# Kernel optimization log

Measured on AMD Instinct MI355X. Metric: run time of the kernel, lower is better.

The kernel has to match this reference:

```python
import jax, jax.numpy as jnp
import numpy as np

B, D_IN, D_OUT, DICT = 2048, 768, 768, 24576
TOP_K, TOP_K_AUX = 32, 512
L1_COEFF, AUX_PENALTY, N_DEAD = 0.001, 0.03125, 100.0


def setup_inputs() -> dict:
    key = jax.random.key(0)
    k1, k2, k3, k4, k5, k6 = jax.random.split(key, 6)
    x_in = jax.random.normal(k1, (B, D_IN), dtype=jnp.float32)
    y_target = jax.random.normal(k2, (B, D_OUT), dtype=jnp.float32)
    nb = jax.random.randint(k3, (DICT,), 0, 200).astype(jnp.float32)
    # kaiming-uniform-ish init
    bound_e = float(np.sqrt(6.0 / D_IN))
    W_enc = jax.random.uniform(k4, (D_IN, DICT), minval=-bound_e, maxval=bound_e, dtype=jnp.float32)
    bound_d = float(np.sqrt(6.0 / DICT))
    W_dec = jax.random.uniform(k5, (DICT, D_OUT), minval=-bound_d, maxval=bound_d, dtype=jnp.float32)
    W_dec = W_dec / jnp.linalg.norm(W_dec, axis=-1, keepdims=True)  # unit-norm rows
    b_dec = jnp.zeros((D_OUT,), dtype=jnp.float32)
    return {"x_in": x_in, "y_target": y_target, "num_batches_not_active": nb,
            "W_enc": W_enc, "W_dec": W_dec, "b_dec": b_dec}


def _unit_norm(x):
    m = x.mean(axis=-1, keepdims=True)
    x = x - m
    s = jnp.std(x, axis=-1, keepdims=True, ddof=1)  # torch .std is unbiased
    return x / (s + 1e-5), m, s


def reference(x_in, y_target, num_batches_not_active, W_enc, W_dec, b_dec):
    xn, _, _ = _unit_norm(x_in)
    yn, y_mean, y_std = _unit_norm(y_target)
    x_enc = xn - b_dec  # pre_enc_bias (input_size == output_size)
    acts = jax.nn.relu(x_enc @ W_enc)                      # [B, DICT]
    vals, idx = jax.lax.top_k(acts, TOP_K)                 # [B, TOP_K]
    rows = jnp.arange(B)[:, None]
    acts_sparse = jnp.zeros_like(acts).at[rows, idx].set(vals)
    y_pred = acts_sparse @ W_dec + b_dec                   # [B, D_OUT]
    y_pred_out = y_pred * y_std + y_mean

    # stateful dead-feature bookkeeping (update_inactive_features)
    col_active = acts_sparse.sum(axis=0) > 0
    nb = jnp.where(col_active, 0.0, num_batches_not_active + 1.0)

    l2_loss = jnp.mean((y_pred - yn) ** 2)
    l1_norm = jnp.mean(jnp.abs(acts_sparse).sum(axis=-1))
    l1_loss = L1_COEFF * l1_norm
    l0_norm = jnp.mean((acts_sparse > 0).astype(jnp.float32).sum(axis=-1))

    # auxiliary loss on dead features (static-shape masked top-k; masked cols
    # get -1 < relu acts so extras relu-clip to 0 -> same math as torch gather)
    dead = nb >= N_DEAD
    masked = jnp.where(dead[None, :], acts, -1.0)
    av, ai = jax.lax.top_k(masked, TOP_K_AUX)
    av = jax.nn.relu(av)
    acts_aux = jnp.zeros_like(acts).at[rows, ai].set(av)
    y_pred_aux = acts_aux @ W_dec
    residual = yn - y_pred
    l2_aux = AUX_PENALTY * jnp.mean((y_pred_aux - residual) ** 2)
    aux_loss = jnp.where(dead.any(), l2_aux, 0.0)

    loss = l2_loss + l1_loss + aux_loss
    num_dead_features = (nb > N_DEAD).sum()
    return (y_pred_out, acts_sparse, loss, l2_loss, l1_loss, l0_norm, l1_norm,
            aux_loss, num_dead_features)
```

## Files before the change

### kernel.cpp

```cpp
#include <hip/hip_runtime.h>
#include <math.h>

#define BATCH 2048
#define DIN 768
#define DICT 24576
#define KM 32
#define KA 512
#define NPT 48
#define L1_COEFF 0.001f
#define AUX_PENALTY 0.03125f
#define CAND_MAX 128
#define CAND_DELTA 0.08f
#define AUX_SPLIT 8
#define SAUX 18432
#define AGB ((DIN/128)*(BATCH/128)*AUX_SPLIT)

typedef __attribute__((ext_vector_type(8))) short bf16x8;
typedef __attribute__((ext_vector_type(8))) unsigned short u16x8;
typedef __attribute__((ext_vector_type(4))) float f32x4;

constexpr size_t WS_XENC   = 0;
constexpr size_t WS_YN     = WS_XENC + (size_t)BATCH*DIN;
constexpr size_t WS_YMEAN  = WS_YN + (size_t)BATCH*DIN;
constexpr size_t WS_YSTD   = WS_YMEAN + BATCH;
constexpr size_t WS_RES    = WS_YSTD + BATCH;
constexpr size_t WS_NSEL   = WS_RES + (size_t)BATCH*DIN;
constexpr size_t WS_SEL    = WS_NSEL + BATCH;
constexpr size_t WS_SELV   = WS_SEL + (size_t)BATCH*KM;
constexpr size_t WS_COLACT = WS_SELV + (size_t)BATCH*KM;
constexpr size_t WS_ACC    = WS_COLACT + DICT;
constexpr size_t WS_DB     = WS_ACC + 8;
constexpr size_t WS_XEB    = WS_DB + DICT/32;
constexpr size_t WS_WETF   = WS_XEB + (size_t)BATCH*DIN/2;
constexpr size_t WS_WETB   = WS_WETF + (size_t)DICT*DIN;
constexpr size_t WS_WDB    = WS_WETB + (size_t)DICT*DIN/2;
constexpr size_t WS_DPREF  = WS_XEB + DICT/32;
constexpr size_t WS_META   = WS_XEB + 2*(DICT/32);

__device__ __forceinline__ unsigned short f2b(float f){
    unsigned u = __float_as_uint(f);
    return (unsigned short)((u + 0x7fffu + ((u >> 16) & 1u)) >> 16);
}
__device__ __forceinline__ float b2f(unsigned short h){ return __uint_as_float(((unsigned)h) << 16); }

__device__ __forceinline__ void gld_lds16(const void* g, void* l){
    __builtin_amdgcn_global_load_lds(
        (const __attribute__((address_space(1))) unsigned int*)g,
        (__attribute__((address_space(3))) unsigned int*)l, 16, 0, 0);
}

__device__ __forceinline__ int blk_count512_w(int cw, int* s16, int par){
    if ((threadIdx.x & 63) == 0) s16[par*8 + (threadIdx.x >> 6)] = cw;
    __syncthreads();
    int tot = 0;
    #pragma unroll
    for (int w=0; w<8; w++) tot += s16[par*8+w];
    return tot;
}
__device__ __forceinline__ float blk_sum512(float v, float* s16, int par){
    #pragma unroll
    for (int off=32; off; off>>=1) v += __shfl_down(v, off);
    if ((threadIdx.x & 63) == 0) s16[par*8 + (threadIdx.x >> 6)] = v;
    __syncthreads();
    float t = 0.f;
    #pragma unroll
    for (int w=0; w<8; w++) t += s16[par*8+w];
    return t;
}
__device__ __forceinline__ float blk_sum256(float v, float* s8, int par){
    #pragma unroll
    for (int off=32; off; off>>=1) v += __shfl_down(v, off);
    if ((threadIdx.x & 63) == 0) s8[par*4 + (threadIdx.x >> 6)] = v;
    __syncthreads();
    float t = 0.f;
    #pragma unroll
    for (int w=0; w<4; w++) t += s8[par*4+w];
    return t;
}

__global__ __launch_bounds__(256) void prep_k(const float* __restrict__ x,
        const float* __restrict__ y, const float* __restrict__ bdec,
        const float* __restrict__ We, const float* __restrict__ Wd,
        float* __restrict__ Tf, unsigned short* __restrict__ Tb,
        unsigned short* __restrict__ Td, float* __restrict__ ws){
    __shared__ float s8[8];
    __shared__ float t1[32][33];
    __shared__ float t2[32][33];
    const int tid = threadIdx.x;
    if (blockIdx.x < 2*BATCH){
        int b = blockIdx.x; bool isy = b >= BATCH; int row = isy ? b - BATCH : b;
        if (b < 8){
            float* dst = ws + WS_COLACT;
            for (int i = b*256 + tid; i < DICT + 8; i += 2048) dst[i] = 0.f;
        }
        const float* src = (isy ? y : x) + (size_t)row*DIN;
        float v0 = src[tid], v1 = src[tid+256], v2 = src[tid+512];
        float s = blk_sum256(v0+v1+v2, s8, 0);
        float mean = s * (1.f/(float)DIN);
        float d0 = v0-mean, d1 = v1-mean, d2 = v2-mean;
        float vs = blk_sum256(d0*d0+d1*d1+d2*d2, s8, 1);
        float sd = sqrtf(vs / (float)(DIN-1));
        float inv = 1.f / (sd + 1e-5f);
        if (isy){
            float* yn = ws + WS_YN + (size_t)row*DIN;
            yn[tid] = d0*inv; yn[tid+256] = d1*inv; yn[tid+512] = d2*inv;
            if (tid==0){ ws[WS_YMEAN+row] = mean; ws[WS_YSTD+row] = sd; }
        } else {
            float* xe = ws + WS_XENC + (size_t)row*DIN;
            unsigned short* xeb = (unsigned short*)(ws + WS_XEB) + (size_t)row*DIN;
            float e0 = d0*inv - bdec[tid];
            float e1 = d1*inv - bdec[tid+256];
            float e2 = d2*inv - bdec[tid+512];
            xe[tid] = e0; xe[tid+256] = e1; xe[tid+512] = e2;
            xeb[tid] = f2b(e0); xeb[tid+256] = f2b(e1); xeb[tid+512] = f2b(e2);
        }
    } else {
        int t = blockIdx.x - 2*BATCH;
        int bx = t % (DICT/32), by = t / (DICT/32);
        int a0 = bx*32, k0 = by*32;
        int r = tid >> 5, c = tid & 31;
        #pragma unroll
        for (int rr=r; rr<32; rr+=8){
            t1[rr][c] = We[(size_t)(k0+rr)*DICT + a0 + c];
            t2[rr][c] = Wd[(size_t)(a0+rr)*DIN + k0 + c];
        }
        __syncthreads();
        #pragma unroll
        for (int rr=r; rr<32; rr+=8){
            float v = t1[c][rr];
            Tf[(size_t)(a0+rr)*DIN + k0 + c] = v;
            Tb[(size_t)(a0+rr)*DIN + k0 + c] = f2b(v);
            Td[(size_t)(k0+rr)*DICT + a0 + c] = f2b(t2[c][rr]);
        }
    }
}

__global__ __launch_bounds__(256) void gemm_mfma(const unsigned short* __restrict__ Abf,
        const unsigned short* __restrict__ Bbf, unsigned short* __restrict__ C){
    __shared__ __align__(16) unsigned short As[128*64];
    __shared__ __align__(16) unsigned short Bs[128*64];
    const int tid = threadIdx.x;
    const int w = tid >> 6, lane = tid & 63;
    const int g = blockIdx.x;
    const int xcd = g & 7;
    const int s_ = g >> 3;
    const int m_t = s_ & 15;
    const int n_t = xcd + 8*(s_ >> 4);
    const int m0 = m_t*128, n0 = n_t*128;
    const int srow = lane >> 3;
    const int schunk = (lane & 7) ^ srow;
    const int wm = (w >> 1)*64, wn = (w & 1)*64;
    f32x4 acc[16];
    #pragma unroll
    for (int i=0;i<16;i++) acc[i] = (f32x4){0.f,0.f,0.f,0.f};
    for (int kt = 0; kt < DIN; kt += 64){
        #pragma unroll
        for (int q=0;q<4;q++){
            int s = w*4 + q;
            int row = 8*s + srow;
            gld_lds16(Abf + (size_t)(m0+row)*DIN + kt + schunk*8, &As[8*s*64]);
            gld_lds16(Bbf + (size_t)(n0+row)*DIN + kt + schunk*8, &Bs[8*s*64]);
        }
        __syncthreads();
        #pragma unroll
        for (int kk=0; kk<64; kk+=32){
            bf16x8 af[4], bfr[4];
            int ch = (kk>>3) + (lane>>4);
            #pragma unroll
            for (int i=0;i<4;i++){
                int row = wm + i*16 + (lane&15);
                af[i] = *(const bf16x8*)&As[row*64 + ((ch ^ (row&7))<<3)];
            }
            #pragma unroll
            for (int j=0;j<4;j++){
                int row = wn + j*16 + (lane&15);
                bfr[j] = *(const bf16x8*)&Bs[row*64 + ((ch ^ (row&7))<<3)];
            }
            #pragma unroll
            for (int i=0;i<4;i++)
                #pragma unroll
                for (int j=0;j<4;j++)
                    acc[i*4+j] = __builtin_amdgcn_mfma_f32_16x16x32_bf16(af[i], bfr[j], acc[i*4+j], 0,0,0);
        }
        __syncthreads();
    }
    #pragma unroll
    for (int i=0;i<4;i++){
        #pragma unroll
        for (int r=0;r<4;r++){
            int m = m0 + wm + i*16 + (lane>>4)*4 + r;
            unsigned short* crow = C + (size_t)m*DICT + n0 + wn + (lane&15);
            #pragma unroll
            for (int j=0;j<4;j++)
                crow[j*16] = f2b(fmaxf(acc[i*4+j][r], 0.f) + 0.0f);
        }
    }
}

__global__ __launch_bounds__(512) void topk_main(const unsigned short* __restrict__ actsb,
        const float* __restrict__ WeTf, const float* __restrict__ Wdec,
        const float* __restrict__ bdec, float* __restrict__ ws,
        float* __restrict__ ypred_out){
    const int row = blockIdx.x, tid = threadIdx.x;
    const int lane = tid & 63, wid = tid >> 6;
    __shared__ int   s_i16[16];
    __shared__ float s_f16[16];
    __shared__ float s_x[DIN];
    __shared__ int   s_ci[CAND_MAX];
    __shared__ float s_cv[CAND_MAX];
    __shared__ int   s_li[KM];
    __shared__ float s_lv[KM];
    __shared__ int   s_n, s_m;
    const unsigned short* arow = actsb + (size_t)row * DICT;
    float* xrow = ws + WS_XENC + (size_t)row * DIN;
    unsigned short h[NPT];
    #pragma unroll
    for (int i=0;i<6;i++){
        u16x8 v = *(const u16x8*)&arow[i*4096 + tid*8];
        #pragma unroll
        for (int e=0;e<8;e++) h[i*8+e] = v[e];
    }
    s_x[tid] = xrow[tid];
    if (tid < DIN-512) s_x[tid+512] = xrow[tid+512];
    if (tid == 0){ s_n = 0; s_m = 0; }

    int par = 0;
    unsigned prefix = 0;
    for (int bit=14; bit>=0; bit--){
        unsigned cand = prefix | (1u<<bit);
        int c = 0;
        #pragma unroll
        for (int q=0;q<NPT;q++) c += (int)__popcll(__ballot((unsigned)h[q] >= cand));
        int tot = blk_count512_w(c, s_i16, par); par ^= 1;
        if (tot >= KM) prefix = cand;
    }
    float tc = b2f((unsigned short)prefix) - CAND_DELTA;
    #pragma unroll
    for (int q=0;q<NPT;q++){
        if (b2f(h[q]) > tc){
            int p = atomicAdd(&s_n, 1);
            if (p < CAND_MAX) s_ci[p] = (q>>3)*4096 + tid*8 + (q&7);
        }
    }
    __syncthreads();
    int nc = s_n; if (nc > CAND_MAX) nc = CAND_MAX;
    for (int c = wid; c < nc; c += 8){
        const float* wr = WeTf + (size_t)s_ci[c]*DIN;
        float p = 0.f;
        #pragma unroll
        for (int t=0; t<12; t++) p = fmaf(s_x[lane + 64*t], wr[lane + 64*t], p);
        #pragma unroll
        for (int off=32; off; off>>=1) p += __shfl_down(p, off);
        if (lane == 0) s_cv[c] = fmaxf(p, 0.f);
    }
    __syncthreads();
    if (tid < nc){
        float vi = s_cv[tid]; int ii = s_ci[tid];
        int rank = 0;
        for (int j=0; j<nc; j++){
            float vj = s_cv[j];
            rank += (vj > vi) || (vj == vi && s_ci[j] < ii);
        }
        if (rank < KM){
            int p = atomicAdd(&s_m, 1);
            s_li[p] = ii; s_lv[p] = vi;
        }
    }
    __syncthreads();
    if (tid < KM){
        ((int*)ws)[WS_COLACT + s_li[tid]] = 1;
        ((int*)ws)[WS_SEL  + (size_t)row*KM + tid] = s_li[tid];
        ws[WS_SELV + (size_t)row*KM + tid] = s_lv[tid];
    }
    if (tid == 0){
        float l1 = 0.f; int l0 = 0;
        for (int l=0;l<KM;l++){ l1 += s_lv[l]; l0 += (s_lv[l] > 0.f); }
        atomicAdd(&ws[WS_ACC+1], l1);
        atomicAdd(&ws[WS_ACC+2], (float)l0);
    }
    __syncthreads();
    float ym = ws[WS_YMEAN+row], ys = ws[WS_YSTD+row];
    float l2loc = 0.f;
    for (int c = tid; c < DIN; c += 512){
        float acc = bdec[c];
        #pragma unroll 4
        for (int l=0;l<KM;l++) acc = fmaf(s_lv[l], Wdec[(size_t)s_li[l]*DIN + c], acc);
        float ynv = ws[WS_YN + (size_t)row*DIN + c];
        float d = acc - ynv;
        l2loc += d*d;
        ws[WS_RES + (size_t)row*DIN + c] = ynv - acc;
        ypred_out[(size_t)row*DIN + c] = fmaf(acc, ys, ym);
        xrow[c] = 0.f;
    }
    if (tid < DIN-512) xrow[tid+512] = 0.f;
    float l2t = blk_sum512(l2loc, s_f16, 0);
    if (tid==0) atomicAdd(&ws[WS_ACC+0], l2t);
}

__global__ __launch_bounds__(768) void deadscan_k(const float* __restrict__ nb,
        float* __restrict__ ws){
    __shared__ int s[DICT/32];
    __shared__ int c12[12];
    const int t = threadIdx.x;
    const int* colact = (const int*)ws + WS_COLACT;
    unsigned bits = 0; int cgt = 0;
    const int base = t*32;
    #pragma unroll 8
    for (int b=0;b<32;b++){
        int j = base + b;
        float nbn = colact[j] ? 0.f : nb[j] + 1.f;
        bits |= (nbn >= 100.f ? 1u : 0u) << b;
        cgt  += (nbn > 100.f) ? 1 : 0;
    }
    ((unsigned*)(ws + WS_DB))[t] = bits;
    int pc = __popc(bits);
    s[t] = pc;
    #pragma unroll
    for (int off=32; off; off>>=1) cgt += __shfl_down(cgt, off);
    if ((t & 63) == 0) c12[t >> 6] = cgt;
    __syncthreads();
    for (int off=1; off<DICT/32; off<<=1){
        int v = (t >= off) ? s[t-off] : 0;
        __syncthreads();
        s[t] += v;
        __syncthreads();
    }
    ((int*)(ws + WS_DPREF))[t] = s[t] - pc;
    if (t == DICT/32 - 1){
        int nd = s[t];
        int ndpad = (nd + 63) & ~63;
        if (ndpad > SAUX) ndpad = SAUX;
        int* meta = (int*)(ws + WS_META);
        meta[0] = nd; meta[1] = ndpad; meta[2] = ndpad >> 6;
        meta[3] = ((ndpad >> 6) + AUX_SPLIT - 1) / AUX_SPLIT;
        int tot = 0;
        #pragma unroll
        for (int wv=0; wv<12; wv++) tot += c12[wv];
        ws[WS_ACC+4] = (float)tot;
        ((int*)ws)[WS_ACC+5] = (nd > 0) ? 1 : 0;
    }
}

__global__ __launch_bounds__(512) void auxprep_k(const unsigned short* __restrict__ actsb,
        unsigned short* __restrict__ wdt, unsigned short* __restrict__ auxc,
        float* __restrict__ ws){
    __shared__ unsigned s_db[DICT/32];
    __shared__ int      s_dp[DICT/32];
    __shared__ int      s_i16[16];
    const int tid = threadIdx.x;
    for (int i=tid; i<DICT/32; i+=512){
        s_db[i] = ((const unsigned*)(ws + WS_DB))[i];
        s_dp[i] = ((const int*)(ws + WS_DPREF))[i];
    }
    const int nd    = ((const int*)(ws + WS_META))[0];
    const int ndpad = ((const int*)(ws + WS_META))[1];
    __syncthreads();
    if (blockIdx.x < DIN){
        const int n = blockIdx.x;
        unsigned short* row = wdt + (size_t)n*DICT;
        for (int ch = 0; ch < DICT; ch += 4096){
            u16x8 a = *(const u16x8*)&row[ch + tid*8];
            __syncthreads();
            int w = (ch>>5) + (tid>>2);
            unsigned dbw = s_db[w]; int dpw = s_dp[w];
            int bit0 = (tid&3)*8;
            #pragma unroll
            for (int e=0;e<8;e++){
                int bit = bit0 + e;
                if ((dbw >> bit) & 1u)
                    row[dpw + __popc(dbw & ((1u<<bit)-1u))] = a[e];
            }
            __syncthreads();
        }
        for (int t2 = nd + tid; t2 < ndpad; t2 += 512) row[t2] = 0;
    } else {
        const int row = blockIdx.x - DIN;
        const unsigned short* arow = actsb + (size_t)row * DICT;
        unsigned short key[NPT];
        #pragma unroll
        for (int i=0;i<6;i++){
            u16x8 v = *(const u16x8*)&arow[i*4096 + tid*8];
            unsigned dbw = s_db[i*128 + (tid>>2)];
            #pragma unroll
            for (int e=0;e<8;e++){
                unsigned short hv = v[e];
                key[i*8+e] = (((dbw >> ((tid&3)*8 + e)) & 1u) && hv) ? hv : 0;
            }
        }
        int par = 0;
        unsigned prefix = 0;
        for (int bit=14; bit>=0; bit--){
            unsigned cand = prefix | (1u<<bit);
            int c = 0;
            #pragma unroll
            for (int q=0;q<NPT;q++) c += (int)__popcll(__ballot((unsigned)key[q] >= cand));
            int tot = blk_count512_w(c, s_i16, par); par ^= 1;
            if (tot >= KA) prefix = cand;
        }
        unsigned thr = prefix ? prefix : 1u;
        unsigned short* crow = auxc + (size_t)row * SAUX;
        #pragma unroll
        for (int i=0;i<6;i++){
            int w = i*128 + (tid>>2);
            unsigned dbw = s_db[w];
            int dpw = s_dp[w];
            #pragma unroll
            for (int e=0;e<8;e++){
                int bit = (tid&3)*8 + e;
                if ((dbw >> bit) & 1u){
                    int p = dpw + __popc(dbw & ((1u<<bit)-1u));
                    unsigned short kv = key[i*8+e];
                    if (p < SAUX) crow[p] = ((unsigned)kv >= thr) ? kv : (unsigned short)0;
                }
            }
        }
        for (int t2 = nd + tid; t2 < ndpad; t2 += 512) crow[t2] = 0;
    }
}

__global__ __launch_bounds__(256) void auxgz_k(const unsigned short* __restrict__ Abf,
        const unsigned short* __restrict__ Bbf, float* __restrict__ ws,
        float* __restrict__ yaux, float* __restrict__ acts){
    __shared__ __align__(16) unsigned short As[128*64];
    __shared__ __align__(16) unsigned short Bs[128*64];
    const int tid = threadIdx.x;
    if (blockIdx.x >= AGB){
        const int row = blockIdx.x - AGB;
        float4 z = make_float4(0.f,0.f,0.f,0.f);
        float4* arow4 = (float4*)(acts + (size_t)row*DICT);
        #pragma unroll
        for (int i=0;i<24;i++) arow4[tid + 256*i] = z;
        __syncthreads();
        if (tid < KM){
            int j   = ((const int*)ws)[WS_SEL + (size_t)row*KM + tid];
            float v = ws[WS_SELV + (size_t)row*KM + tid];
            (acts + (size_t)row*DICT)[j] = v;
        }
        return;
    }
    const int nkt   = ((const int*)(ws + WS_META))[2];
    const int chunk = ((const int*)(ws + WS_META))[3];
    const int g = blockIdx.x;
    const int z = g & 7;
    const int s_ = g >> 3;
    const int m_t = s_ & 15;
    const int n_t = s_ >> 4;
    int t0 = z * chunk;
    int t1 = t0 + chunk; if (t1 > nkt) t1 = nkt;
    if (t0 >= t1) return;
    const int w = tid >> 6, lane = tid & 63;
    const int m0 = m_t*128, n0 = n_t*128;
    const int srow = lane >> 3;
    const int schunk = (lane & 7) ^ srow;
    const int wm = (w >> 1)*64, wn = (w & 1)*64;
    f32x4 acc[16];
    #pragma unroll
    for (int i=0;i<16;i++) acc[i] = (f32x4){0.f,0.f,0.f,0.f};
    for (int t = t0; t < t1; ++t){
        int kt = t*64;
        #pragma unroll
        for (int q=0;q<4;q++){
            int s = w*4 + q;
            int row = 8*s + srow;
            gld_lds16(Abf + (size_t)(m0+row)*SAUX + kt + schunk*8, &As[8*s*64]);
            gld_lds16(Bbf + (size_t)(n0+row)*DICT + kt + schunk*8, &Bs[8*s*64]);
        }
        __syncthreads();
        #pragma unroll
        for (int kk=0; kk<64; kk+=32){
            bf16x8 af[4], bfr[4];
            int ch = (kk>>3) + (lane>>4);
            #pragma unroll
            for (int i=0;i<4;i++){
                int row = wm + i*16 + (lane&15);
                af[i] = *(const bf16x8*)&As[row*64 + ((ch ^ (row&7))<<3)];
            }
            #pragma unroll
            for (int j=0;j<4;j++){
                int row = wn + j*16 + (lane&15);
                bfr[j] = *(const bf16x8*)&Bs[row*64 + ((ch ^ (row&7))<<3)];
            }
            #pragma unroll
            for (int i=0;i<4;i++)
                #pragma unroll
                for (int j=0;j<4;j++)
                    acc[i*4+j] = __builtin_amdgcn_mfma_f32_16x16x32_bf16(af[i], bfr[j], acc[i*4+j], 0,0,0);
        }
        __syncthreads();
    }
    #pragma unroll
    for (int i=0;i<4;i++){
        #pragma unroll
        for (int r=0;r<4;r++){
            int m = m0 + wm + i*16 + (lane>>4)*4 + r;
            float* crow = yaux + (size_t)m*DIN + n0 + wn + (lane&15);
            #pragma unroll
            for (int j=0;j<4;j++) atomicAdd(&crow[j*16], acc[i*4+j][r]);
        }
    }
}

__global__ __launch_bounds__(256) void auxloss_k(const float* __restrict__ yaux,
        float* __restrict__ ws){
    __shared__ float s8[8];
    const float4* y4 = (const float4*)yaux;
    const float4* r4 = (const float4*)(ws + WS_RES);
    float s = 0.f;
    const size_t n4 = (size_t)BATCH*DIN/4;
    for (size_t i = (size_t)blockIdx.x*256 + threadIdx.x; i < n4; i += (size_t)gridDim.x*256){
        float4 a = y4[i], b = r4[i];
        float d0 = a.x-b.x, d1 = a.y-b.y, d2 = a.z-b.z, d3 = a.w-b.w;
        s += d0*d0 + d1*d1 + d2*d2 + d3*d3;
    }
    float tot = blk_sum256(s, s8, 0);
    if (threadIdx.x == 0) atomicAdd(&ws[WS_ACC+3], tot);
}

__global__ void finalize_k(const float* __restrict__ ws, float* __restrict__ out){
    if (threadIdx.x == 0){
        float l2   = ws[WS_ACC+0] / (float)((size_t)BATCH*DIN);
        float l1n  = ws[WS_ACC+1] / (float)BATCH;
        float l1l  = L1_COEFF * l1n;
        float l0   = ws[WS_ACC+2] / (float)BATCH;
        float auxm = AUX_PENALTY * (ws[WS_ACC+3] / (float)((size_t)BATCH*DIN));
        int any    = ((const int*)ws)[WS_ACC+5];
        float auxl = any ? auxm : 0.f;
        out[0] = l2 + l1l + auxl;
        out[1] = l2;
        out[2] = l1l;
        out[3] = l0;
        out[4] = l1n;
        out[5] = auxl;
        out[6] = ws[WS_ACC+4];
    }
}

extern "C" void kernel_launch(void* const* d_in, const int* in_sizes, int n_in,
                              void* d_out, int out_size, void* d_ws, size_t ws_size,
                              hipStream_t stream){
    const float* x_in = (const float*)d_in[0];
    const float* y_t  = (const float*)d_in[1];
    const float* nb   = (const float*)d_in[2];
    const float* Wenc = (const float*)d_in[3];
    const float* Wdec = (const float*)d_in[4];
    const float* bdec = (const float*)d_in[5];
    float* out  = (float*)d_out;
    float* ws   = (float*)d_ws;
    float* acts = out + (size_t)BATCH*DIN;
    float* scal = out + (size_t)BATCH*DIN + (size_t)BATCH*DICT;
    unsigned short* actsb = (unsigned short*)acts;

    unsigned short* xeb  = (unsigned short*)(ws + WS_XEB);
    float*          wetf = ws + WS_WETF;
    unsigned short* wetb = (unsigned short*)(ws + WS_WETB);
    unsigned short* wdt  = (unsigned short*)(ws + WS_WDB);
    unsigned short* auxc = (unsigned short*)(ws + WS_WETF);
    float*          yaux = ws + WS_XENC;

    prep_k<<<2*BATCH + (DICT/32)*(DIN/32), 256, 0, stream>>>(
        x_in, y_t, bdec, Wenc, Wdec, wetf, wetb, wdt, ws);
    gemm_mfma<<<(DICT/128)*(BATCH/128), 256, 0, stream>>>(xeb, wetb, actsb);
    topk_main<<<BATCH, 512, 0, stream>>>(actsb, wetf, Wdec, bdec, ws, out);
    deadscan_k<<<1, DICT/32, 0, stream>>>(nb, ws);
    auxprep_k<<<DIN + BATCH, 512, 0, stream>>>(actsb, wdt, auxc, ws);
    auxgz_k<<<AGB + BATCH, 256, 0, stream>>>(auxc, wdt, ws, yaux, acts);
    auxloss_k<<<256, 256, 0, stream>>>(yaux, ws);
    finalize_k<<<1, 64, 0, stream>>>(ws, scal);
}
```

Baseline: 858.5 us.

## Stage aux compaction in LDS, replace split-K atomics with partial buffers

The aux GEMM's split-K partial results now go to eight separate workspace buffers with plain stores instead of float atomicAdd. The loss kernel sums the eight partials while reading the residual, which also removes the need to zero the yaux buffer in topk_main. The auxprep compaction of W_dec rows and aux codes is staged in a shared-memory buffer and written out with coalesced vector stores instead of scattered global writes. The main top-k threshold search now counts per wave without a block-wide reduction, and the candidate capacity is raised to 768 to cover the larger candidate set this produces. The cost is more LDS per block and more global traffic in the loss kernel reading eight buffers.

```diff
diff --git a/kernel.cpp b/kernel.cpp
--- a/kernel.cpp
+++ b/kernel.cpp
@@ -9,7 +9,7 @@
 #define NPT 48
 #define L1_COEFF 0.001f
 #define AUX_PENALTY 0.03125f
-#define CAND_MAX 128
+#define CAND_MAX 768
 #define CAND_DELTA 0.08f
 #define AUX_SPLIT 8
 #define SAUX 18432
@@ -203,7 +203,6 @@
         float* __restrict__ ypred_out){
     const int row = blockIdx.x, tid = threadIdx.x;
     const int lane = tid & 63, wid = tid >> 6;
-    __shared__ int   s_i16[16];
     __shared__ float s_f16[16];
     __shared__ float s_x[DIN];
     __shared__ int   s_ci[CAND_MAX];
@@ -212,7 +211,7 @@
     __shared__ float s_lv[KM];
     __shared__ int   s_n, s_m;
     const unsigned short* arow = actsb + (size_t)row * DICT;
-    float* xrow = ws + WS_XENC + (size_t)row * DIN;
+    const float* xrow = ws + WS_XENC + (size_t)row * DIN;
     unsigned short h[NPT];
     #pragma unroll
     for (int i=0;i<6;i++){
@@ -224,17 +223,16 @@
     if (tid < DIN-512) s_x[tid+512] = xrow[tid+512];
     if (tid == 0){ s_n = 0; s_m = 0; }
 
-    int par = 0;
     unsigned prefix = 0;
     for (int bit=14; bit>=0; bit--){
         unsigned cand = prefix | (1u<<bit);
         int c = 0;
         #pragma unroll
         for (int q=0;q<NPT;q++) c += (int)__popcll(__ballot((unsigned)h[q] >= cand));
-        int tot = blk_count512_w(c, s_i16, par); par ^= 1;
-        if (tot >= KM) prefix = cand;
+        if (c >= KM) prefix = cand;
     }
     float tc = b2f((unsigned short)prefix) - CAND_DELTA;
+    __syncthreads();
     #pragma unroll
     for (int q=0;q<NPT;q++){
         if (b2f(h[q]) > tc){
@@ -290,9 +288,7 @@
         l2loc += d*d;
         ws[WS_RES + (size_t)row*DIN + c] = ynv - acc;
         ypred_out[(size_t)row*DIN + c] = fmaf(acc, ys, ym);
-        xrow[c] = 0.f;
-    }
-    if (tid < DIN-512) xrow[tid+512] = 0.f;
+    }
     float l2t = blk_sum512(l2loc, s_f16, 0);
     if (tid==0) atomicAdd(&ws[WS_ACC+0], l2t);
 }
@@ -347,6 +343,7 @@
     __shared__ unsigned s_db[DICT/32];
     __shared__ int      s_dp[DICT/32];
     __shared__ int      s_i16[16];
+    __shared__ unsigned short s_out[SAUX];
     const int tid = threadIdx.x;
     for (int i=tid; i<DICT/32; i+=512){
         s_db[i] = ((const unsigned*)(ws + WS_DB))[i];
@@ -358,21 +355,24 @@
     if (blockIdx.x < DIN){
         const int n = blockIdx.x;
         unsigned short* row = wdt + (size_t)n*DICT;
-        for (int ch = 0; ch < DICT; ch += 4096){
-            u16x8 a = *(const u16x8*)&row[ch + tid*8];
-            __syncthreads();
-            int w = (ch>>5) + (tid>>2);
+        #pragma unroll
+        for (int i=0;i<6;i++){
+            u16x8 a = *(const u16x8*)&row[i*4096 + tid*8];
+            int w = i*128 + (tid>>2);
             unsigned dbw = s_db[w]; int dpw = s_dp[w];
-            int bit0 = (tid&3)*8;
             #pragma unroll
             for (int e=0;e<8;e++){
-                int bit = bit0 + e;
-                if ((dbw >> bit) & 1u)
-                    row[dpw + __popc(dbw & ((1u<<bit)-1u))] = a[e];
-            }
-            __syncthreads();
-        }
-        for (int t2 = nd + tid; t2 < ndpad; t2 += 512) row[t2] = 0;
+                int bit = (tid&3)*8 + e;
+                if ((dbw >> bit) & 1u){
+                    int p = dpw + __popc(dbw & ((1u<<bit)-1u));
+                    if (p < SAUX) s_out[p] = a[e];
+                }
+            }
+        }
+        for (int t2 = nd + tid; t2 < ndpad; t2 += 512) s_out[t2] = 0;
+        __syncthreads();
+        for (int i = tid*8; i < ndpad; i += 4096)
+            *(u16x8*)&row[i] = *(const u16x8*)&s_out[i];
     } else {
         const int row = blockIdx.x - DIN;
         const unsigned short* arow = actsb + (size_t)row * DICT;
@@ -398,7 +398,6 @@
             if (tot >= KA) prefix = cand;
         }
         unsigned thr = prefix ? prefix : 1u;
-        unsigned short* crow = auxc + (size_t)row * SAUX;
         #pragma unroll
         for (int i=0;i<6;i++){
             int w = i*128 + (tid>>2);
@@ -410,17 +409,21 @@
                 if ((dbw >> bit) & 1u){
                     int p = dpw + __popc(dbw & ((1u<<bit)-1u));
                     unsigned short kv = key[i*8+e];
-                    if (p < SAUX) crow[p] = ((unsigned)kv >= thr) ? kv : (unsigned short)0;
+                    if (p < SAUX) s_out[p] = ((unsigned)kv >= thr) ? kv : (unsigned short)0;
                 }
             }
         }
-        for (int t2 = nd + tid; t2 < ndpad; t2 += 512) crow[t2] = 0;
+        for (int t2 = nd + tid; t2 < ndpad; t2 += 512) s_out[t2] = 0;
+        __syncthreads();
+        unsigned short* crow = auxc + (size_t)row * SAUX;
+        for (int i = tid*8; i < ndpad; i += 4096)
+            *(u16x8*)&crow[i] = *(const u16x8*)&s_out[i];
     }
 }
 
 __global__ __launch_bounds__(256) void auxgz_k(const unsigned short* __restrict__ Abf,
         const unsigned short* __restrict__ Bbf, float* __restrict__ ws,
-        float* __restrict__ yaux, float* __restrict__ acts){
+        float* __restrict__ acts){
     __shared__ __align__(16) unsigned short As[128*64];
     __shared__ __align__(16) unsigned short Bs[128*64];
     const int tid = threadIdx.x;
@@ -447,7 +450,6 @@
     const int n_t = s_ >> 4;
     int t0 = z * chunk;
     int t1 = t0 + chunk; if (t1 > nkt) t1 = nkt;
-    if (t0 >= t1) return;
     const int w = tid >> 6, lane = tid & 63;
     const int m0 = m_t*128, n0 = n_t*128;
     const int srow = lane >> 3;
@@ -488,29 +490,42 @@
         }
         __syncthreads();
     }
+    float* buf = ws + ((z < 6) ? (WS_WETB + (size_t)z*BATCH*DIN)
+                               : (z == 6 ? WS_YN : WS_XENC));
     #pragma unroll
     for (int i=0;i<4;i++){
         #pragma unroll
         for (int r=0;r<4;r++){
             int m = m0 + wm + i*16 + (lane>>4)*4 + r;
-            float* crow = yaux + (size_t)m*DIN + n0 + wn + (lane&15);
-            #pragma unroll
-            for (int j=0;j<4;j++) atomicAdd(&crow[j*16], acc[i*4+j][r]);
-        }
-    }
-}
-
-__global__ __launch_bounds__(256) void auxloss_k(const float* __restrict__ yaux,
-        float* __restrict__ ws){
+            float* crow = buf + (size_t)m*DIN + n0 + wn + (lane&15);
+            #pragma unroll
+            for (int j=0;j<4;j++) crow[j*16] = acc[i*4+j][r];
+        }
+    }
+}
+
+__global__ __launch_bounds__(256) void auxloss_k(float* __restrict__ ws){
     __shared__ float s8[8];
-    const float4* y4 = (const float4*)yaux;
+    const float4* b0 = (const float4*)(ws + WS_WETB);
+    const float4* b1 = (const float4*)(ws + WS_WETB + 1*(size_t)BATCH*DIN);
+    const float4* b2 = (const float4*)(ws + WS_WETB + 2*(size_t)BATCH*DIN);
+    const float4* b3 = (const float4*)(ws + WS_WETB + 3*(size_t)BATCH*DIN);
+    const float4* b4 = (const float4*)(ws + WS_WETB + 4*(size_t)BATCH*DIN);
+    const float4* b5 = (const float4*)(ws + WS_WETB + 5*(size_t)BATCH*DIN);
+    const float4* b6 = (const float4*)(ws + WS_YN);
+    const float4* b7 = (const float4*)(ws + WS_XENC);
     const float4* r4 = (const float4*)(ws + WS_RES);
     float s = 0.f;
     const size_t n4 = (size_t)BATCH*DIN/4;
     for (size_t i = (size_t)blockIdx.x*256 + threadIdx.x; i < n4; i += (size_t)gridDim.x*256){
-        float4 a = y4[i], b = r4[i];
-        float d0 = a.x-b.x, d1 = a.y-b.y, d2 = a.z-b.z, d3 = a.w-b.w;
-        s += d0*d0 + d1*d1 + d2*d2 + d3*d3;
+        float4 a0 = b0[i], a1 = b1[i], a2 = b2[i], a3 = b3[i];
+        float4 a4 = b4[i], a5 = b5[i], a6 = b6[i], a7 = b7[i];
+        float4 rr = r4[i];
+        float x0 = ((a0.x+a1.x)+(a2.x+a3.x))+((a4.x+a5.x)+(a6.x+a7.x)) - rr.x;
+        float x1 = ((a0.y+a1.y)+(a2.y+a3.y))+((a4.y+a5.y)+(a6.y+a7.y)) - rr.y;
+        float x2 = ((a0.z+a1.z)+(a2.z+a3.z))+((a4.z+a5.z)+(a6.z+a7.z)) - rr.z;
+        float x3 = ((a0.w+a1.w)+(a2.w+a3.w))+((a4.w+a5.w)+(a6.w+a7.w)) - rr.w;
+        s += x0*x0 + x1*x1 + x2*x2 + x3*x3;
     }
     float tot = blk_sum256(s, s8, 0);
     if (threadIdx.x == 0) atomicAdd(&ws[WS_ACC+3], tot);
@@ -555,7 +570,6 @@
     unsigned short* wetb = (unsigned short*)(ws + WS_WETB);
     unsigned short* wdt  = (unsigned short*)(ws + WS_WDB);
     unsigned short* auxc = (unsigned short*)(ws + WS_WETF);
-    float*          yaux = ws + WS_XENC;
 
     prep_k<<<2*BATCH + (DICT/32)*(DIN/32), 256, 0, stream>>>(
         x_in, y_t, bdec, Wenc, Wdec, wetf, wetb, wdt, ws);
@@ -563,7 +577,7 @@
     topk_main<<<BATCH, 512, 0, stream>>>(actsb, wetf, Wdec, bdec, ws, out);
     deadscan_k<<<1, DICT/32, 0, stream>>>(nb, ws);
     auxprep_k<<<DIN + BATCH, 512, 0, stream>>>(actsb, wdt, auxc, ws);
-    auxgz_k<<<AGB + BATCH, 256, 0, stream>>>(auxc, wdt, ws, yaux, acts);
-    auxloss_k<<<256, 256, 0, stream>>>(yaux, ws);
+    auxgz_k<<<AGB + BATCH, 256, 0, stream>>>(auxc, wdt, ws, acts);
+    auxloss_k<<<256, 256, 0, stream>>>(ws);
     finalize_k<<<1, 64, 0, stream>>>(ws, scal);
 }
```

Result: slower. 1.041 ms (+21.2%).
